# Kernel optimization log

Hardware: AMD Instinct MI355X
Metric: run time of the kernel (lower is better)

## Reference

```python
import jax, jax.numpy as jnp
import numpy as np

B, S, DM = 2, 2048, 1024
H, DH = 16, 64
SCALE = jnp.sqrt(jnp.float32(DH))  # dot_scale = sqrt(dim_head)


def setup_inputs() -> dict:
    key = jax.random.key(0)
    ks = jax.random.split(key, 9)
    std = 1.0 / np.sqrt(DM)
    x = jax.random.normal(ks[0], (B, S, DM), dtype=jnp.float32)
    Wq = jax.random.uniform(ks[1], (DM, DM), jnp.float32, -std, std)
    bq = jax.random.uniform(ks[2], (DM,), jnp.float32, -std, std)
    Wk = jax.random.uniform(ks[3], (DM, DM), jnp.float32, -std, std)
    bk = jax.random.uniform(ks[4], (DM,), jnp.float32, -std, std)
    Wv = jax.random.uniform(ks[5], (DM, DM), jnp.float32, -std, std)
    bv = jax.random.uniform(ks[6], (DM,), jnp.float32, -std, std)
    Wo = jax.random.uniform(ks[7], (DM, DM), jnp.float32, -std, std)
    bo = jax.random.uniform(ks[8], (DM,), jnp.float32, -std, std)
    # causal mask: 1 = masked (future positions), broadcast over batch
    causal = jnp.triu(jnp.ones((S, S), dtype=jnp.int32), k=1)
    attention_mask = jnp.broadcast_to(causal, (B, S, S))
    return {"x": x, "Wq": Wq, "bq": bq, "Wk": Wk, "bk": bk,
            "Wv": Wv, "bv": bv, "Wo": Wo, "bo": bo,
            "attention_mask": attention_mask}


def reference(x, Wq, bq, Wk, bk, Wv, bv, Wo, bo, attention_mask):
    # Linear layers (torch nn.Linear: y = x @ W^T + b)
    q = (x @ Wq.T + bq).reshape(B, S, H, DH).transpose(0, 2, 1, 3)  # (B,H,S,DH)
    k = (x @ Wk.T + bk).reshape(B, S, H, DH).transpose(0, 2, 1, 3)  # (B,H,S,DH)
    v = (x @ Wv.T + bv).reshape(B, S, H, DH).transpose(0, 2, 1, 3)  # (B,H,S,DH)
    # scores: (B,H,S,S), then mask==1 -> -inf, softmax over last dim
    scores = jnp.einsum('bhsd,bhtd->bhst', q, k) / SCALE
    mask = attention_mask[:, None, :, :]  # (B,1,S,S)
    scores = jnp.where(mask == 1, -jnp.inf, scores)
    attn = jax.nn.softmax(scores, axis=-1)
    # dropout is identity in eval mode
    ctx = jnp.einsum('bhst,bhtd->bshd', attn, v).reshape(B, S, H * DH)
    return ctx @ Wo.T + bo
```

## Files before the change

### kernel.cpp

```cpp
#include <hip/hip_runtime.h>
#include <stdint.h>

typedef unsigned short u16;
typedef __attribute__((ext_vector_type(8))) short bf16x8;
typedef __attribute__((ext_vector_type(4))) float f32x4;

#define BATCH 2
#define S_LEN 2048
#define DMODEL 1024
#define NH 16
#define DHEAD 64
#define MTOT 4096
#define QSCALE 0.18033688011112042f

#define GL2LDS(g, l) \
  __builtin_amdgcn_global_load_lds((const __attribute__((address_space(1))) void*)(g), \
                                   (__attribute__((address_space(3))) void*)(l), 16, 0, 0)

__device__ __forceinline__ u16 f2bf(float x) {
  union { float f; uint32_t u; } v; v.f = x;
  uint32_t r = v.u + 0x7fffu + ((v.u >> 16) & 1u);
  return (u16)(r >> 16);
}
__device__ __forceinline__ u16 f2bf_fast(float x) {
  union { float f; uint32_t u; } v; v.f = x;
  return (u16)((v.u + 0x8000u) >> 16);
}

struct CvtArgs {
  const float* src[5];
  u16* dst[5];
};

__global__ __launch_bounds__(256) void cvt_all(CvtArgs a) {
  int bx = blockIdx.x;
  int region, off;
  if (bx < 4096) { region = 0; off = bx; }
  else { region = 1 + ((bx - 4096) >> 10); off = (bx - 4096) & 1023; }
  const float* s = a.src[region];
  u16* d = a.dst[region];
  int i = (off * 256 + threadIdx.x) * 4;
  float4 v = *(const float4*)(s + i);
  uint2 pk;
  pk.x = (uint32_t)f2bf(v.x) | ((uint32_t)f2bf(v.y) << 16);
  pk.y = (uint32_t)f2bf(v.z) | ((uint32_t)f2bf(v.w) << 16);
  *(uint2*)(d + i) = pk;
}

__device__ __forceinline__ void gemm_body(const u16* __restrict__ A,
                                          const u16* __restrict__ W,
                                          const float* __restrict__ bias,
                                          void* __restrict__ out,
                                          int mode, float scale) {
  __shared__ u16 As[128 * 32];
  __shared__ u16 Bs[128 * 32];
  const int tid = threadIdx.x;
  const int m0 = blockIdx.y * 128;
  const int n0 = blockIdx.x * 128;
  const int wave = tid >> 6, lane = tid & 63;
  const int wm = (wave >> 1) * 64, wn = (wave & 1) * 64;
  const int quad = lane >> 4, l15 = lane & 15;

  const int row0 = tid >> 2, g0 = ((tid & 3) ^ (row0 & 3)) * 8;
  const int row1 = (tid + 256) >> 2, g1 = ((tid & 3) ^ (row1 & 3)) * 8;
  const int lb0 = wave * 512;
  const int lb1 = 2048 + wave * 512;
  const int xk = (quad ^ (l15 & 3)) * 8;

  f32x4 acc[4][4] = {};

  for (int kt = 0; kt < DMODEL; kt += 32) {
    GL2LDS(A + (size_t)(m0 + row0) * DMODEL + kt + g0, As + lb0);
    GL2LDS(A + (size_t)(m0 + row1) * DMODEL + kt + g1, As + lb1);
    GL2LDS(W + (size_t)(n0 + row0) * DMODEL + kt + g0, Bs + lb0);
    GL2LDS(W + (size_t)(n0 + row1) * DMODEL + kt + g1, Bs + lb1);
    __syncthreads();
    bf16x8 af[4], bfr[4];
#pragma unroll
    for (int bi = 0; bi < 4; ++bi)
      af[bi] = *(const bf16x8*)(&As[(wm + bi * 16 + l15) * 32 + xk]);
#pragma unroll
    for (int bj = 0; bj < 4; ++bj)
      bfr[bj] = *(const bf16x8*)(&Bs[(wn + bj * 16 + l15) * 32 + xk]);
#pragma unroll
    for (int bi = 0; bi < 4; ++bi)
#pragma unroll
      for (int bj = 0; bj < 4; ++bj)
        acc[bi][bj] = __builtin_amdgcn_mfma_f32_16x16x32_bf16(af[bi], bfr[bj], acc[bi][bj], 0, 0, 0);
    __syncthreads();
  }

#pragma unroll
  for (int bi = 0; bi < 4; ++bi) {
#pragma unroll
    for (int bj = 0; bj < 4; ++bj) {
      int n = n0 + wn + bj * 16 + l15;
      float bval = bias[n];
#pragma unroll
      for (int r = 0; r < 4; ++r) {
        int m = m0 + wm + bi * 16 + quad * 4 + r;
        float v = (acc[bi][bj][r] + bval) * scale;
        u16 bvu = f2bf(v);
        int b = m >> 11, s = m & 2047;
        int h = n >> 6, d = n & 63;
        size_t bh = (size_t)(b * NH + h);
        if (mode == 1)
          ((u16*)out)[(bh * S_LEN + s) * DHEAD + d] = bvu;
        else
          ((u16*)out)[((bh * 256 + (s >> 3)) * 64 + d) * 8 + (s & 7)] = bvu;
      }
    }
  }
}

struct QKVArgs {
  const u16* w[3];
  const float* b[3];
  u16* o[3];
};

__global__ __launch_bounds__(256) void qkv_gemm(const u16* __restrict__ xb, QKVArgs a) {
  int z = blockIdx.z;
  int mode = (z == 2) ? 2 : 1;
  float scale = (z == 0) ? QSCALE : 1.0f;
  gemm_body(xb, a.w[z], a.b[z], a.o[z], mode, scale);
}

__global__ __launch_bounds__(256) void out_gemm(const u16* __restrict__ A,
                                                const u16* __restrict__ W,
                                                const float* __restrict__ bias,
                                                float* __restrict__ out) {
  __shared__ u16 As[128 * 32];
  __shared__ u16 Bs[64 * 32];
  const int tid = threadIdx.x;
  const int m0 = blockIdx.y * 128;
  const int n0 = blockIdx.x * 64;
  const int wave = tid >> 6, lane = tid & 63;
  const int wm = (wave >> 1) * 64, wn = (wave & 1) * 32;
  const int quad = lane >> 4, l15 = lane & 15;

  const int row0 = tid >> 2, g0 = ((tid & 3) ^ (row0 & 3)) * 8;
  const int row1 = (tid + 256) >> 2, g1 = ((tid & 3) ^ (row1 & 3)) * 8;
  const int lb0 = wave * 512;
  const int lb1 = 2048 + wave * 512;
  const int xk = (quad ^ (l15 & 3)) * 8;

  f32x4 acc[4][2] = {};

  for (int kt = 0; kt < DMODEL; kt += 32) {
    GL2LDS(A + (size_t)(m0 + row0) * DMODEL + kt + g0, As + lb0);
    GL2LDS(A + (size_t)(m0 + row1) * DMODEL + kt + g1, As + lb1);
    GL2LDS(W + (size_t)(n0 + row0) * DMODEL + kt + g0, Bs + lb0);
    __syncthreads();
    bf16x8 af[4], bfr[2];
#pragma unroll
    for (int bi = 0; bi < 4; ++bi)
      af[bi] = *(const bf16x8*)(&As[(wm + bi * 16 + l15) * 32 + xk]);
#pragma unroll
    for (int bj = 0; bj < 2; ++bj)
      bfr[bj] = *(const bf16x8*)(&Bs[(wn + bj * 16 + l15) * 32 + xk]);
#pragma unroll
    for (int bi = 0; bi < 4; ++bi)
#pragma unroll
      for (int bj = 0; bj < 2; ++bj)
        acc[bi][bj] = __builtin_amdgcn_mfma_f32_16x16x32_bf16(af[bi], bfr[bj], acc[bi][bj], 0, 0, 0);
    __syncthreads();
  }

#pragma unroll
  for (int bi = 0; bi < 4; ++bi) {
#pragma unroll
    for (int bj = 0; bj < 2; ++bj) {
      int n = n0 + wn + bj * 16 + l15;
      float bval = bias[n];
#pragma unroll
      for (int r = 0; r < 4; ++r) {
        int m = m0 + wm + bi * 16 + quad * 4 + r;
        out[(size_t)m * DMODEL + n] = acc[bi][bj][r] + bval;
      }
    }
  }
}

__global__ __launch_bounds__(256) void attn(const u16* __restrict__ Q,
                                            const u16* __restrict__ Kg,
                                            const u16* __restrict__ Vt8,
                                            u16* __restrict__ ctx) {
  __shared__ u16 Kd[2][128 * 64];
  __shared__ u16 Vd[2][64 * 128];
  __shared__ u16 Ps[64 * 80];
  const int tid = threadIdx.x;
  const int qp = blockIdx.x >> 5;
  const int bh = blockIdx.x & 31;
  const int wave = tid >> 6, lane = tid & 63;
  const int quad = lane >> 4, l15 = lane & 15;
  const size_t base = (size_t)bh * S_LEN * DHEAD;
  const int b = bh >> 4, h = bh & 15;
  const int xk7 = l15 & 7;

#define STAGE(kt_, pb)                                                                   \
  do {                                                                                   \
    _Pragma("unroll")                                                                    \
    for (int i_ = 0; i_ < 4; ++i_) {                                                     \
      int c_ = tid + 256 * i_;                                                           \
      int row_ = c_ >> 3, g_ = ((c_ & 7) ^ (row_ & 7)) * 8;                              \
      GL2LDS(Kg + base + (size_t)((kt_) * 128 + row_) * 64 + g_,                         \
             &Kd[pb][0] + i_ * 2048 + wave * 512);                                       \
      GL2LDS(Vt8 + base + (size_t)((kt_) * 1024 + c_) * 8,                               \
             &Vd[pb][0] + i_ * 2048 + wave * 512);                                       \
    }                                                                                    \
  } while (0)

  for (int half = 0; half < 2; ++half) {
    const int qt = half ? (31 - qp) : qp;
    const int qrow = qt * 64 + wave * 16 + l15;
    bf16x8 qf0 = *(const bf16x8*)(Q + base + (size_t)qrow * DHEAD + quad * 8);
    bf16x8 qf1 = *(const bf16x8*)(Q + base + (size_t)qrow * DHEAD + 32 + quad * 8);

    float l_part[4] = {0.f, 0.f, 0.f, 0.f};
    f32x4 o[4] = {};

    const int ktmax = qt >> 1;
    STAGE(0, 0);

    for (int kt = 0; kt <= ktmax; ++kt) {
      const int p = kt & 1;
      __syncthreads();
      if (kt < ktmax) STAGE(kt + 1, p ^ 1);

      const bool diag = (kt == ktmax);
      const int qg_max = qt * 64 + wave * 16 + 15;
      f32x4 s_acc[8];
#pragma unroll
      for (int bj = 0; bj < 8; ++bj) {
        if (diag && (kt * 128 + bj * 16 > qg_max)) {
          s_acc[bj] = f32x4{-1e30f, -1e30f, -1e30f, -1e30f};
          continue;
        }
        const int krow = (bj * 16 + l15) * 64;
        bf16x8 kf0 = *(const bf16x8*)(&Kd[p][krow + ((quad ^ xk7) * 8)]);
        bf16x8 kf1 = *(const bf16x8*)(&Kd[p][krow + (((quad + 4) ^ xk7) * 8)]);
        f32x4 t = {0.f, 0.f, 0.f, 0.f};
        t = __builtin_amdgcn_mfma_f32_16x16x32_bf16(qf0, kf0, t, 0, 0, 0);
        t = __builtin_amdgcn_mfma_f32_16x16x32_bf16(qf1, kf1, t, 0, 0, 0);
        s_acc[bj] = t;
      }

      if (diag) {
#pragma unroll
        for (int bj = 0; bj < 8; ++bj) {
          int kg = kt * 128 + bj * 16 + l15;
#pragma unroll
          for (int r = 0; r < 4; ++r) {
            int qg = qt * 64 + wave * 16 + quad * 4 + r;
            if (kg > qg) s_acc[bj][r] = -1e30f;
          }
        }
      }

#pragma unroll
      for (int ph = 0; ph < 2; ++ph) {
        if (diag && (kt * 128 + ph * 64 > qg_max)) continue;
#pragma unroll
        for (int bj2 = 0; bj2 < 4; ++bj2) {
          int bj = ph * 4 + bj2;
#pragma unroll
          for (int r = 0; r < 4; ++r) {
            float pv = exp2f(s_acc[bj][r]);
            l_part[r] += pv;
            Ps[(wave * 16 + quad * 4 + r) * 80 + bj2 * 16 + l15] = f2bf_fast(pv);
          }
        }
#pragma unroll
        for (int kk2 = 0; kk2 < 2; ++kk2) {
          bf16x8 pf = *(const bf16x8*)(&Ps[(wave * 16 + l15) * 80 + kk2 * 32 + quad * 8]);
          int kk = ph * 2 + kk2;
#pragma unroll
          for (int dj = 0; dj < 4; ++dj) {
            bf16x8 vf = *(const bf16x8*)(&Vd[p][((kk * 4 + quad) * 64 + dj * 16 + l15) * 8]);
            o[dj] = __builtin_amdgcn_mfma_f32_16x16x32_bf16(pf, vf, o[dj], 0, 0, 0);
          }
        }
      }
    }

    __syncthreads();

#pragma unroll
    for (int r = 0; r < 4; ++r) {
      float s = l_part[r];
      s += __shfl_xor(s, 1, 64);
      s += __shfl_xor(s, 2, 64);
      s += __shfl_xor(s, 4, 64);
      s += __shfl_xor(s, 8, 64);
      float inv = 1.0f / s;
      int srow = qt * 64 + wave * 16 + quad * 4 + r;
      size_t rowbase = ((size_t)b * S_LEN + srow) * DMODEL + h * DHEAD;
#pragma unroll
      for (int dj = 0; dj < 4; ++dj)
        ctx[rowbase + dj * 16 + l15] = f2bf(o[dj][r] * inv);
    }
  }
#undef STAGE
}

extern "C" void kernel_launch(void* const* d_in, const int* in_sizes, int n_in,
                              void* d_out, int out_size, void* d_ws, size_t ws_size,
                              hipStream_t stream) {
  const float* x  = (const float*)d_in[0];
  const float* Wq = (const float*)d_in[1];
  const float* bq = (const float*)d_in[2];
  const float* Wk = (const float*)d_in[3];
  const float* bk = (const float*)d_in[4];
  const float* Wv = (const float*)d_in[5];
  const float* bv = (const float*)d_in[6];
  const float* Wo = (const float*)d_in[7];
  const float* bo = (const float*)d_in[8];
  float* out = (float*)d_out;

  char* ws = (char*)d_ws;
  const size_t MB = 1u << 20;
  u16* xb   = (u16*)(ws + 0);
  u16* ctxb = xb;
  u16* wqb  = (u16*)(ws + 8 * MB);
  u16* wkb  = (u16*)(ws + 10 * MB);
  u16* wvb  = (u16*)(ws + 12 * MB);
  u16* wob  = (u16*)(ws + 14 * MB);
  u16* qb   = (u16*)(ws + 16 * MB);
  u16* kb   = (u16*)(ws + 24 * MB);
  u16* vtb  = (u16*)(ws + 32 * MB);

  CvtArgs c;
  c.src[0] = x;  c.dst[0] = xb;
  c.src[1] = Wq; c.dst[1] = wqb;
  c.src[2] = Wk; c.dst[2] = wkb;
  c.src[3] = Wv; c.dst[3] = wvb;
  c.src[4] = Wo; c.dst[4] = wob;
  cvt_all<<<4096 + 4 * 1024, 256, 0, stream>>>(c);

  QKVArgs a;
  a.w[0] = wqb; a.w[1] = wkb; a.w[2] = wvb;
  a.b[0] = bq;  a.b[1] = bk;  a.b[2] = bv;
  a.o[0] = qb;  a.o[1] = kb;  a.o[2] = vtb;
  qkv_gemm<<<dim3(DMODEL / 128, MTOT / 128, 3), 256, 0, stream>>>(xb, a);

  attn<<<512, 256, 0, stream>>>(qb, kb, vtb, ctxb);

  out_gemm<<<dim3(DMODEL / 64, MTOT / 128), 256, 0, stream>>>(ctxb, wob, bo, out);
}
```

Baseline: 209.2 us.

## Share K/V tile loads between paired query tiles in causal attention

Each block previously handled two query tiles (qp and 31-qp) one after the other, streaming K/V from global memory twice. Both tiles now run in a single key loop, so every staged K/V tile in LDS serves both query tiles and global K/V traffic and barriers drop by roughly a third. The P scratch row stride is reduced from 80 to 72 and launch bounds request two blocks per CU. In exchange, each thread holds two sets of Q fragments and accumulators, which raises register pressure, and the Ps buffer is reused back to back between the two tiles.

```diff
diff --git a/kernel.cpp b/kernel.cpp
--- a/kernel.cpp
+++ b/kernel.cpp
@@ -12,6 +12,7 @@
 #define DHEAD 64
 #define MTOT 4096
 #define QSCALE 0.18033688011112042f
+#define PST 72
 
 #define GL2LDS(g, l) \
   __builtin_amdgcn_global_load_lds((const __attribute__((address_space(1))) void*)(g), \
@@ -182,13 +183,76 @@
   }
 }
 
-__global__ __launch_bounds__(256) void attn(const u16* __restrict__ Q,
-                                            const u16* __restrict__ Kg,
-                                            const u16* __restrict__ Vt8,
-                                            u16* __restrict__ ctx) {
+__device__ __forceinline__ void attn_tile(int qt, int kt, int km,
+                                          bf16x8 qf0, bf16x8 qf1,
+                                          float* l_part, f32x4* o,
+                                          const u16* __restrict__ K,
+                                          const u16* __restrict__ V,
+                                          u16* __restrict__ Ps,
+                                          int wave, int quad, int l15, int xk7) {
+  const bool diag = (kt == km);
+  const int qg_max = qt * 64 + wave * 16 + 15;
+  f32x4 s_acc[8];
+#pragma unroll
+  for (int bj = 0; bj < 8; ++bj) {
+    if (diag && (kt * 128 + bj * 16 > qg_max)) {
+      s_acc[bj] = f32x4{-1e30f, -1e30f, -1e30f, -1e30f};
+      continue;
+    }
+    const int krow = (bj * 16 + l15) * 64;
+    bf16x8 kf0 = *(const bf16x8*)(&K[krow + ((quad ^ xk7) * 8)]);
+    bf16x8 kf1 = *(const bf16x8*)(&K[krow + (((quad + 4) ^ xk7) * 8)]);
+    f32x4 t = {0.f, 0.f, 0.f, 0.f};
+    t = __builtin_amdgcn_mfma_f32_16x16x32_bf16(qf0, kf0, t, 0, 0, 0);
+    t = __builtin_amdgcn_mfma_f32_16x16x32_bf16(qf1, kf1, t, 0, 0, 0);
+    s_acc[bj] = t;
+  }
+
+  if (diag) {
+#pragma unroll
+    for (int bj = 0; bj < 8; ++bj) {
+      int kg = kt * 128 + bj * 16 + l15;
+#pragma unroll
+      for (int r = 0; r < 4; ++r) {
+        int qg = qt * 64 + wave * 16 + quad * 4 + r;
+        if (kg > qg) s_acc[bj][r] = -1e30f;
+      }
+    }
+  }
+
+#pragma unroll
+  for (int ph = 0; ph < 2; ++ph) {
+    if (diag && (kt * 128 + ph * 64 > qg_max)) continue;
+#pragma unroll
+    for (int bj2 = 0; bj2 < 4; ++bj2) {
+      int bj = ph * 4 + bj2;
+#pragma unroll
+      for (int r = 0; r < 4; ++r) {
+        float pv = exp2f(s_acc[bj][r]);
+        l_part[r] += pv;
+        Ps[(wave * 16 + quad * 4 + r) * PST + bj2 * 16 + l15] = f2bf_fast(pv);
+      }
+    }
+#pragma unroll
+    for (int kk2 = 0; kk2 < 2; ++kk2) {
+      bf16x8 pf = *(const bf16x8*)(&Ps[(wave * 16 + l15) * PST + kk2 * 32 + quad * 8]);
+      int kk = ph * 2 + kk2;
+#pragma unroll
+      for (int dj = 0; dj < 4; ++dj) {
+        bf16x8 vf = *(const bf16x8*)(&V[((kk * 4 + quad) * 64 + dj * 16 + l15) * 8]);
+        o[dj] = __builtin_amdgcn_mfma_f32_16x16x32_bf16(pf, vf, o[dj], 0, 0, 0);
+      }
+    }
+  }
+}
+
+__global__ __launch_bounds__(256, 2) void attn(const u16* __restrict__ Q,
+                                               const u16* __restrict__ Kg,
+                                               const u16* __restrict__ Vt8,
+                                               u16* __restrict__ ctx) {
   __shared__ u16 Kd[2][128 * 64];
   __shared__ u16 Vd[2][64 * 128];
-  __shared__ u16 Ps[64 * 80];
+  __shared__ u16 Ps[64 * PST];
   const int tid = threadIdx.x;
   const int qp = blockIdx.x >> 5;
   const int bh = blockIdx.x & 31;
@@ -211,84 +275,40 @@
     }                                                                                    \
   } while (0)
 
-  for (int half = 0; half < 2; ++half) {
-    const int qt = half ? (31 - qp) : qp;
-    const int qrow = qt * 64 + wave * 16 + l15;
-    bf16x8 qf0 = *(const bf16x8*)(Q + base + (size_t)qrow * DHEAD + quad * 8);
-    bf16x8 qf1 = *(const bf16x8*)(Q + base + (size_t)qrow * DHEAD + 32 + quad * 8);
-
-    float l_part[4] = {0.f, 0.f, 0.f, 0.f};
-    f32x4 o[4] = {};
-
-    const int ktmax = qt >> 1;
-    STAGE(0, 0);
-
-    for (int kt = 0; kt <= ktmax; ++kt) {
-      const int p = kt & 1;
-      __syncthreads();
-      if (kt < ktmax) STAGE(kt + 1, p ^ 1);
-
-      const bool diag = (kt == ktmax);
-      const int qg_max = qt * 64 + wave * 16 + 15;
-      f32x4 s_acc[8];
-#pragma unroll
-      for (int bj = 0; bj < 8; ++bj) {
-        if (diag && (kt * 128 + bj * 16 > qg_max)) {
-          s_acc[bj] = f32x4{-1e30f, -1e30f, -1e30f, -1e30f};
-          continue;
-        }
-        const int krow = (bj * 16 + l15) * 64;
-        bf16x8 kf0 = *(const bf16x8*)(&Kd[p][krow + ((quad ^ xk7) * 8)]);
-        bf16x8 kf1 = *(const bf16x8*)(&Kd[p][krow + (((quad + 4) ^ xk7) * 8)]);
-        f32x4 t = {0.f, 0.f, 0.f, 0.f};
-        t = __builtin_amdgcn_mfma_f32_16x16x32_bf16(qf0, kf0, t, 0, 0, 0);
-        t = __builtin_amdgcn_mfma_f32_16x16x32_bf16(qf1, kf1, t, 0, 0, 0);
-        s_acc[bj] = t;
-      }
-
-      if (diag) {
-#pragma unroll
-        for (int bj = 0; bj < 8; ++bj) {
-          int kg = kt * 128 + bj * 16 + l15;
-#pragma unroll
-          for (int r = 0; r < 4; ++r) {
-            int qg = qt * 64 + wave * 16 + quad * 4 + r;
-            if (kg > qg) s_acc[bj][r] = -1e30f;
-          }
-        }
-      }
-
-#pragma unroll
-      for (int ph = 0; ph < 2; ++ph) {
-        if (diag && (kt * 128 + ph * 64 > qg_max)) continue;
-#pragma unroll
-        for (int bj2 = 0; bj2 < 4; ++bj2) {
-          int bj = ph * 4 + bj2;
-#pragma unroll
-          for (int r = 0; r < 4; ++r) {
-            float pv = exp2f(s_acc[bj][r]);
-            l_part[r] += pv;
-            Ps[(wave * 16 + quad * 4 + r) * 80 + bj2 * 16 + l15] = f2bf_fast(pv);
-          }
-        }
-#pragma unroll
-        for (int kk2 = 0; kk2 < 2; ++kk2) {
-          bf16x8 pf = *(const bf16x8*)(&Ps[(wave * 16 + l15) * 80 + kk2 * 32 + quad * 8]);
-          int kk = ph * 2 + kk2;
-#pragma unroll
-          for (int dj = 0; dj < 4; ++dj) {
-            bf16x8 vf = *(const bf16x8*)(&Vd[p][((kk * 4 + quad) * 64 + dj * 16 + l15) * 8]);
-            o[dj] = __builtin_amdgcn_mfma_f32_16x16x32_bf16(pf, vf, o[dj], 0, 0, 0);
-          }
-        }
-      }
-    }
-
-    __syncthreads();
-
+  const int qtA = qp, qtB = 31 - qp;
+  const int kmA = qtA >> 1, kmB = qtB >> 1;
+
+  const int qrowA = qtA * 64 + wave * 16 + l15;
+  const int qrowB = qtB * 64 + wave * 16 + l15;
+  bf16x8 qfA0 = *(const bf16x8*)(Q + base + (size_t)qrowA * DHEAD + quad * 8);
+  bf16x8 qfA1 = *(const bf16x8*)(Q + base + (size_t)qrowA * DHEAD + 32 + quad * 8);
+  bf16x8 qfB0 = *(const bf16x8*)(Q + base + (size_t)qrowB * DHEAD + quad * 8);
+  bf16x8 qfB1 = *(const bf16x8*)(Q + base + (size_t)qrowB * DHEAD + 32 + quad * 8);
+
+  float lA[4] = {0.f, 0.f, 0.f, 0.f}, lB[4] = {0.f, 0.f, 0.f, 0.f};
+  f32x4 oA[4] = {}, oB[4] = {};
+
+  STAGE(0, 0);
+  for (int kt = 0; kt <= kmB; ++kt) {
+    const int p = kt & 1;
+    __syncthreads();
+    if (kt < kmB) STAGE(kt + 1, p ^ 1);
+
+    if (kt <= kmA)
+      attn_tile(qtA, kt, kmA, qfA0, qfA1, lA, oA, &Kd[p][0], &Vd[p][0], Ps,
+                wave, quad, l15, xk7);
+    attn_tile(qtB, kt, kmB, qfB0, qfB1, lB, oB, &Kd[p][0], &Vd[p][0], Ps,
+              wave, quad, l15, xk7);
+  }
+
+#pragma unroll
+  for (int e = 0; e < 2; ++e) {
+    const int qt = e ? qtB : qtA;
+    float* lp = e ? lB : lA;
+    f32x4* op = e ? oB : oA;
 #pragma unroll
     for (int r = 0; r < 4; ++r) {
-      float s = l_part[r];
+      float s = lp[r];
       s += __shfl_xor(s, 1, 64);
       s += __shfl_xor(s, 2, 64);
       s += __shfl_xor(s, 4, 64);
@@ -298,7 +318,7 @@
       size_t rowbase = ((size_t)b * S_LEN + srow) * DMODEL + h * DHEAD;
 #pragma unroll
       for (int dj = 0; dj < 4; ++dj)
-        ctx[rowbase + dj * 16 + l15] = f2bf(o[dj][r] * inv);
+        ctx[rowbase + dj * 16 + l15] = f2bf(op[dj][r] * inv);
     }
   }
 #undef STAGE
```

Result: no change. 212.9 us (+1.8%).
